# Kernel tuning notes

Measured on AMD Instinct MI355X. Metric: run time of the kernel, lower is better.

The kernel has to match this reference:

```python
import jax, jax.numpy as jnp
import numpy as np

B, L, V, D, N, K = 8, 512, 50257, 1024, 1024, 256


def setup_inputs() -> dict:
    key = jax.random.key(0)
    ks = jax.random.split(key, 8)
    s = 0.02
    return {
        "input_ids": jax.random.randint(ks[0], (B, L), 0, V, dtype=jnp.int32),
        "emb_inp": jax.random.normal(ks[1], (V, D), jnp.float32) * s,
        "W_ih": jax.random.normal(ks[2], (3 * D, D), jnp.float32) * s,   # rows ordered [r|z|n] like torch GRU
        "W_hh": jax.random.normal(ks[3], (3 * D, D), jnp.float32) * s,
        "b_ih": jnp.zeros((3 * D,), jnp.float32),
        "b_hh": jnp.zeros((3 * D,), jnp.float32),
        "W_A": jax.random.normal(ks[4], (N * K, D), jnp.float32) * s,    # ctx_to_A weight
        "b_A": jnp.zeros((N * K,), jnp.float32),
        "emb_geom": jax.random.normal(ks[5], (V, N), jnp.float32) * s,
    }


def reference(input_ids, emb_inp, W_ih, W_hh, b_ih, b_hh, W_A, b_A, emb_geom):
    # token embedding: (B, L, D)
    x = emb_inp[input_ids]
    # precompute input-side GRU gates once: (B, L, 3D)
    gi = jnp.einsum('bld,gd->blg', x, W_ih) + b_ih

    def step(h, gi_t):
        gh = h @ W_hh.T + b_hh                       # (B, 3D)
        ir, iz, i_n = jnp.split(gi_t, 3, axis=-1)
        hr, hz, h_n = jnp.split(gh, 3, axis=-1)
        r = jax.nn.sigmoid(ir + hr)
        z = jax.nn.sigmoid(iz + hz)
        n = jnp.tanh(i_n + r * h_n)
        h_new = (1.0 - z) * n + z * h                # torch GRU update
        return h_new, None

    h0 = jnp.zeros((x.shape[0], D), x.dtype)
    ctx_vec, _ = jax.lax.scan(step, h0, jnp.swapaxes(gi, 0, 1))  # final hidden (B, D)

    # context -> subspace basis U: (B, n, k)
    U = (ctx_vec @ W_A.T + b_A).reshape(-1, N, K)

    # scores[b,v] = e_v^T (U U^T) e_v == ||U^T e_v||^2  (rank-k rewrite, same math)
    Ue = jnp.einsum('vn,bnk->bvk', emb_geom, U)      # (B, V, K)
    logits = jnp.sum(Ue * Ue, axis=-1)               # (B, V)
    return logits
```

## Files before the change

### kernel.cpp

```cpp
#include <hip/hip_runtime.h>

#define D 1024
#define G3 3072
#define NV 50257
#define NU 1024
#define KU 256
#define TOKROWS 4096
#define SCL 256.0f
#define ISCL2 (1.0f / 65536.0f)
#define ISCL4 (1.0f / 4294967296.0f)

typedef __attribute__((ext_vector_type(8))) _Float16 half8;
typedef __attribute__((ext_vector_type(4))) _Float16 half4;
typedef __attribute__((ext_vector_type(4))) float f32x4;
typedef __attribute__((ext_vector_type(4))) unsigned u32x4;

#define GLDS16(gp, lp) __builtin_amdgcn_global_load_lds( \
    (const __attribute__((address_space(1))) void*)(const void*)(gp), \
    (__attribute__((address_space(3))) void*)(void*)(lp), 16, 0, 0)

static __device__ __forceinline__ float sigmoidf_(float x) {
  return 1.0f / (1.0f + __expf(-x));
}
static __device__ __forceinline__ float tanhf_(float x) {
  float e = __expf(2.0f * x);
  return 1.0f - 2.0f / (e + 1.0f);
}

__global__ __launch_bounds__(256) void k_prep(
    const int* __restrict__ ids, const float* __restrict__ emb,
    const float* __restrict__ Wih,
    _Float16* __restrict__ xh, _Float16* __restrict__ xl,
    _Float16* __restrict__ wh, _Float16* __restrict__ wl)
{
  int t = threadIdx.x;
  int wg = blockIdx.x;
  const float* src;
  _Float16 *dh, *dl;
  if (wg < TOKROWS) {
    src = emb + (size_t)ids[wg] * D;
    dh = xh + (size_t)wg * D; dl = xl + (size_t)wg * D;
  } else {
    int r = wg - TOKROWS;
    src = Wih + (size_t)r * D;
    dh = wh + (size_t)r * D; dl = wl + (size_t)r * D;
  }
  f32x4 v = ((const f32x4*)src)[t];
  half4 h, l;
#pragma unroll
  for (int j = 0; j < 4; ++j) {
    float vs = v[j] * SCL;
    _Float16 hi = (_Float16)vs;
    h[j] = hi;
    l[j] = (_Float16)(vs - (float)hi);
  }
  *(half4*)(dh + t * 4) = h;
  *(half4*)(dl + t * 4) = l;
}

__global__ __launch_bounds__(256) void k_gi(
    const _Float16* __restrict__ Ah, const _Float16* __restrict__ Al,
    const _Float16* __restrict__ Bh, const _Float16* __restrict__ Bl,
    const float* __restrict__ bih, float* __restrict__ gi)
{
  __shared__ _Float16 Ash[128 * 64];
  __shared__ _Float16 Asl[128 * 64];
  __shared__ _Float16 Bsh[128 * 64];
  __shared__ _Float16 Bsl[128 * 64];
  int tid = threadIdx.x;
  int bm = blockIdx.x, bn = blockIdx.y;
  int lane = tid & 63, w = tid >> 6;
  int nl = lane & 15, q = lane >> 4;
  int wr = w >> 1, wc = w & 1;
  f32x4 zero = {0.f, 0.f, 0.f, 0.f};
  f32x4 acc[4][4];
#pragma unroll
  for (int i = 0; i < 4; i++)
#pragma unroll
    for (int j = 0; j < 4; j++) acc[i][j] = zero;
  int srow_in = tid >> 3;
  int cg = ((tid & 7) ^ (srow_in & 7)) * 8;
  for (int kc = 0; kc < 16; ++kc) {
    __syncthreads();
#pragma unroll
    for (int s = 0; s < 4; ++s) {
      size_t go = ((size_t)(bm * 128 + s * 32 + srow_in)) * D + kc * 64 + cg;
      size_t go2 = ((size_t)(bn * 128 + s * 32 + srow_in)) * D + kc * 64 + cg;
      int lb = s * 2048 + w * 512;
      GLDS16(Ah + go, Ash + lb);
      GLDS16(Al + go, Asl + lb);
      GLDS16(Bh + go2, Bsh + lb);
      GLDS16(Bl + go2, Bsl + lb);
    }
    __syncthreads();
    half8 afh[4][2], afl[4][2], bfh[4][2], bfl[4][2];
#pragma unroll
    for (int mt = 0; mt < 4; ++mt) {
      int R = wr * 64 + mt * 16 + nl;
#pragma unroll
      for (int kt = 0; kt < 2; ++kt) {
        int o = R * 64 + ((kt * 4 + q) ^ (R & 7)) * 8;
        afh[mt][kt] = *(const half8*)(Ash + o);
        afl[mt][kt] = *(const half8*)(Asl + o);
      }
    }
#pragma unroll
    for (int nt = 0; nt < 4; ++nt) {
      int R = wc * 64 + nt * 16 + nl;
#pragma unroll
      for (int kt = 0; kt < 2; ++kt) {
        int o = R * 64 + ((kt * 4 + q) ^ (R & 7)) * 8;
        bfh[nt][kt] = *(const half8*)(Bsh + o);
        bfl[nt][kt] = *(const half8*)(Bsl + o);
      }
    }
#pragma unroll
    for (int mt = 0; mt < 4; ++mt)
#pragma unroll
      for (int nt = 0; nt < 4; ++nt)
#pragma unroll
        for (int kt = 0; kt < 2; ++kt) {
          acc[mt][nt] = __builtin_amdgcn_mfma_f32_16x16x32_f16(afh[mt][kt], bfh[nt][kt], acc[mt][nt], 0, 0, 0);
          acc[mt][nt] = __builtin_amdgcn_mfma_f32_16x16x32_f16(afh[mt][kt], bfl[nt][kt], acc[mt][nt], 0, 0, 0);
          acc[mt][nt] = __builtin_amdgcn_mfma_f32_16x16x32_f16(afl[mt][kt], bfh[nt][kt], acc[mt][nt], 0, 0, 0);
        }
  }
#pragma unroll
  for (int mt = 0; mt < 4; ++mt)
#pragma unroll
    for (int nt = 0; nt < 4; ++nt) {
      int col = bn * 128 + wc * 64 + nt * 16 + nl;
      float bv = bih[col];
#pragma unroll
      for (int i = 0; i < 4; i++) {
        int row = bm * 128 + wr * 64 + mt * 16 + q * 4 + i;
        gi[(size_t)row * G3 + col] = acc[mt][nt][i] * ISCL2 + bv;
      }
    }
}

__global__ void k_init(unsigned* __restrict__ rec32)
{
  int t = threadIdx.x;
  for (int i = t; i < 32768; i += 256) rec32[i] = 0u;
}

__global__ __launch_bounds__(384) void k_gru(
    const float* __restrict__ Whh, const float* __restrict__ gi,
    const float* __restrict__ bhh, unsigned* __restrict__ hrec,
    float* __restrict__ ctx)
{
  int tid = threadIdx.x;
  int wid = blockIdx.x;
  int w = tid >> 6;
  int g = w >> 1;
  int kh = w & 1;
  int lane = tid & 63, nl = lane & 15, q = lane >> 4;
  __shared__ _Float16 hs[16 * 1024];
  __shared__ float gp[6][3][8][17];

  half8 bwh[16], bwl[16];
  {
    const float* wrow = Whh + ((size_t)(g * 1024 + wid * 16 + nl)) * D + kh * 512;
#pragma unroll
    for (int kt = 0; kt < 16; ++kt) {
      const f32x4* p = (const f32x4*)(wrow + kt * 32 + q * 8);
      f32x4 v0 = p[0], v1 = p[1];
      half8 h, l;
#pragma unroll
      for (int j = 0; j < 4; ++j) {
        float s0 = v0[j] * SCL;
        _Float16 h0 = (_Float16)s0;
        h[j] = h0; l[j] = (_Float16)(s0 - (float)h0);
        float s1 = v1[j] * SCL;
        _Float16 h1 = (_Float16)s1;
        h[j + 4] = h1; l[j + 4] = (_Float16)(s1 - (float)h1);
      }
      bwh[kt] = h; bwl[kt] = l;
    }
  }

  int m = tid >> 3, np = (tid & 7) * 2;
  int d0 = wid * 16 + np;
  float hr0 = 0.f, hr1 = 0.f;
  float bh[6] = {0, 0, 0, 0, 0, 0};
  if (tid < 64) {
#pragma unroll
    for (int gg = 0; gg < 3; ++gg) {
      bh[gg * 2] = bhh[gg * 1024 + d0];
      bh[gg * 2 + 1] = bhh[gg * 1024 + d0 + 1];
    }
  }
  f32x4 zero = {0, 0, 0, 0};

  for (int step = 0; step < 512; ++step) {
    float gi6[6] = {0, 0, 0, 0, 0, 0};
    if (tid < 64) {
      const float* gpt = gi + ((size_t)(m * 512 + step)) * G3 + d0;
#pragma unroll
      for (int gg = 0; gg < 3; ++gg) {
        gi6[gg * 2] = gpt[gg * 1024];
        gi6[gg * 2 + 1] = gpt[gg * 1024 + 1];
      }
    }

    {
      unsigned want = (unsigned)step;
      const u32x4* rb = (const u32x4*)hrec + (size_t)(step & 1) * 4096;
      u32x4 rv[11];
      unsigned need = 0;
#pragma unroll
      for (int k = 0; k < 11; ++k) {
        int r = tid + k * 384;
        if (r < 4096) need |= (1u << k);
      }
      while (need) {
        unsigned mm = need;
#pragma unroll
        for (int k = 0; k < 11; ++k)
          if (mm & (1u << k)) {
            int r = tid + k * 384;
            asm volatile("global_load_dwordx4 %0, %1, off sc0 sc1"
                         : "=v"(rv[k]) : "v"(rb + r));
          }
        asm volatile("s_waitcnt vmcnt(0)" ::: "memory");
#pragma unroll
        for (int k = 0; k < 11; ++k)
          if ((mm & (1u << k)) && rv[k][2] == want) need &= ~(1u << k);
      }
      __builtin_amdgcn_sched_barrier(0);
#pragma unroll
      for (int k = 0; k < 11; ++k) {
        int r = tid + k * 384;
        if (r < 4096) {
          int w2 = r >> 6, l2 = r & 63;
          int m2 = l2 >> 3;
          int d = (w2 << 4) + ((l2 & 7) << 1);
          int chunk = d >> 3, wi = d & 7;
          int sw = chunk ^ (m2 & 7);
          *(unsigned*)&hs[((m2 * 128 + sw) << 3) + wi] = rv[k][0];
          *(unsigned*)&hs[(((m2 + 8) * 128 + sw) << 3) + wi] = rv[k][1];
        }
      }
    }
    __syncthreads();

    half8 av[16];
#pragma unroll
    for (int kt = 0; kt < 16; ++kt) {
      int chunk = kh * 64 + kt * 4 + q;
      av[kt] = *(const half8*)&hs[(size_t)(nl * 128 + (chunk ^ (nl & 7))) * 8];
    }
    f32x4 ac1 = zero, ac2 = zero;
#pragma unroll
    for (int kt = 0; kt < 16; ++kt) {
      ac1 = __builtin_amdgcn_mfma_f32_16x16x32_f16(av[kt], bwh[kt], ac1, 0, 0, 0);
      ac2 = __builtin_amdgcn_mfma_f32_16x16x32_f16(av[kt], bwl[kt], ac2, 0, 0, 0);
    }
    if (q < 2) {
#pragma unroll
      for (int i = 0; i < 4; i++) {
        gp[w][0][q * 4 + i][nl] = ac1[i];
        gp[w][2][q * 4 + i][nl] = ac2[i];
      }
    } else {
#pragma unroll
      for (int i = 0; i < 4; i++) gp[w][1][(q - 2) * 4 + i][nl] = ac1[i];
    }
    __syncthreads();
    if (tid < 64) {
      float gh[6];
#pragma unroll
      for (int g2 = 0; g2 < 3; ++g2) {
        float s0 = 0.f, s1 = 0.f;
#pragma unroll
        for (int k2 = 0; k2 < 2; ++k2) {
          int wv = g2 * 2 + k2;
#pragma unroll
          for (int s = 0; s < 3; ++s) {
            s0 += gp[wv][s][m][np];
            s1 += gp[wv][s][m][np + 1];
          }
        }
        gh[g2 * 2] = s0 * ISCL2;
        gh[g2 * 2 + 1] = s1 * ISCL2;
      }
      float r0_ = sigmoidf_(gi6[0] + gh[0] + bh[0]);
      float r1_ = sigmoidf_(gi6[1] + gh[1] + bh[1]);
      float z0_ = sigmoidf_(gi6[2] + gh[2] + bh[2]);
      float z1_ = sigmoidf_(gi6[3] + gh[3] + bh[3]);
      float n0_ = tanhf_(gi6[4] + r0_ * (gh[4] + bh[4]));
      float n1_ = tanhf_(gi6[5] + r1_ * (gh[5] + bh[5]));
      float h0_ = (1.f - z0_) * n0_ + z0_ * hr0;
      float h1_ = (1.f - z1_) * n1_ + z1_ * hr1;
      hr0 = h0_; hr1 = h1_;
      float s0 = h0_ * SCL, s1 = h1_ * SCL;
      _Float16 h0h = (_Float16)s0, h1h = (_Float16)s1;
      _Float16 h0l = (_Float16)(s0 - (float)h0h), h1l = (_Float16)(s1 - (float)h1h);
      u32x4 rec;
      rec[0] = (unsigned)__builtin_bit_cast(unsigned short, h0h) |
               ((unsigned)__builtin_bit_cast(unsigned short, h1h) << 16);
      rec[1] = (unsigned)__builtin_bit_cast(unsigned short, h0l) |
               ((unsigned)__builtin_bit_cast(unsigned short, h1l) << 16);
      rec[2] = (unsigned)(step + 1);
      rec[3] = 0u;
      u32x4* dst = (u32x4*)hrec + ((size_t)((step + 1) & 1) * 4096 + wid * 64 + tid);
      asm volatile("global_store_dwordx4 %0, %1, off sc0 sc1"
                   :: "v"(dst), "v"(rec) : "memory");
      if (step == 511) {
        ctx[m * D + d0] = h0_;
        ctx[m * D + d0 + 1] = h1_;
      }
    }
  }
}

__global__ __launch_bounds__(256) void k_u(
    const float* __restrict__ WA, const float* __restrict__ bA,
    const float* __restrict__ ctx, _Float16* __restrict__ Uth,
    _Float16* __restrict__ Utl)
{
  __shared__ float As[128 * 32];
  __shared__ float cx[8][1032];
  int tid = threadIdx.x;
  int RB = blockIdx.x;
#pragma unroll
  for (int jj = 0; jj < 8; ++jj) {
    int e = tid * 32 + jj * 4;
    *(f32x4*)&cx[e >> 10][e & 1023] = *(const f32x4*)(ctx + e);
  }
  float acc[4] = {0.f, 0.f, 0.f, 0.f};
  int b = tid & 7, rq = tid >> 3;
  float* AsW = As + (tid >> 6) * 256;
  int sr = tid >> 3;
  int sc = (tid & 7) * 4;
  __syncthreads();
  for (int kc = 0; kc < 32; ++kc) {
    __syncthreads();
    const float* gsrc = WA + ((size_t)(RB * 128 + sr)) * D + kc * 32 + sc;
    GLDS16(gsrc, AsW);
    GLDS16(gsrc + 32 * D, AsW + 1024);
    GLDS16(gsrc + 64 * D, AsW + 2048);
    GLDS16(gsrc + 96 * D, AsW + 3072);
    __syncthreads();
    f32x4 cxr[8];
#pragma unroll
    for (int kk = 0; kk < 8; ++kk) cxr[kk] = *(const f32x4*)&cx[b][kc * 32 + kk * 4];
#pragma unroll
    for (int r = 0; r < 4; ++r) {
      const float* ap = As + (rq * 4 + r) * 32;
      float s = 0.f;
#pragma unroll
      for (int kk = 0; kk < 8; ++kk) {
        f32x4 a = *(const f32x4*)(ap + kk * 4);
        f32x4 c = cxr[kk];
        s += a[0] * c[0] + a[1] * c[1] + a[2] * c[2] + a[3] * c[3];
      }
      acc[r] += s;
    }
  }
#pragma unroll
  for (int r = 0; r < 4; ++r) {
    int R = RB * 128 + rq * 4 + r;
    float v = (acc[r] + bA[R]) * SCL;
    int n_u = R >> 8, k_u = R & 255;
    _Float16 hi = (_Float16)v;
    size_t o = ((size_t)(b * 256 + k_u)) * NU + n_u;
    Uth[o] = hi;
    Utl[o] = (_Float16)(v - (float)hi);
  }
}

__global__ __launch_bounds__(512, 1) void k_logits(
    const float* __restrict__ eg, const _Float16* __restrict__ Uth,
    const _Float16* __restrict__ Utl, float* __restrict__ out)
{
  __shared__ _Float16 Ash[128 * 40];
  __shared__ _Float16 Asl[128 * 40];
  __shared__ float lacc[8][128];
  int tid = threadIdx.x;
  int v0 = blockIdx.x * 128;
  int lane = tid & 63, w = tid >> 6, nl = lane & 15, q = lane >> 4;
  int bh = w & 1, wk = w >> 1;
  for (int i = tid; i < 1024; i += 512) ((float*)lacc)[i] = 0.f;
  int sr = tid >> 2;
  int sc = (tid & 3) * 8;
  int vr = v0 + sr;
  if (vr >= NV) vr = NV - 1;
  const float* asrc = eg + (size_t)vr * NU;
  f32x4 zero = {0, 0, 0, 0};
  f32x4 u0 = *(const f32x4*)(asrc + sc);
  f32x4 u1 = *(const f32x4*)(asrc + sc + 4);
  __syncthreads();
  for (int kg = 0; kg < 4; ++kg) {
    f32x4 acc[4][8];
#pragma unroll
    for (int b = 0; b < 4; ++b)
#pragma unroll
      for (int mt = 0; mt < 8; ++mt) acc[b][mt] = zero;
    for (int nc = 0; nc < 32; ++nc) {
      __syncthreads();
      {
        half8 h, l;
#pragma unroll
        for (int j = 0; j < 4; ++j) {
          float s0 = u0[j] * SCL;
          _Float16 h0 = (_Float16)s0;
          h[j] = h0; l[j] = (_Float16)(s0 - (float)h0);
          float s1 = u1[j] * SCL;
          _Float16 h1 = (_Float16)s1;
          h[j + 4] = h1; l[j + 4] = (_Float16)(s1 - (float)h1);
        }
        *(half8*)(Ash + sr * 40 + sc) = h;
        *(half8*)(Asl + sr * 40 + sc) = l;
      }
      {
        int nnc = (nc + 1) & 31;
        const f32x4* np_ = (const f32x4*)(asrc + nnc * 32 + sc);
        u0 = np_[0];
        u1 = np_[1];
      }
      __syncthreads();
      half8 afh[8], afl[8];
#pragma unroll
      for (int mt = 0; mt < 8; ++mt) {
        afh[mt] = *(const half8*)(Ash + (mt * 16 + nl) * 40 + q * 8);
        afl[mt] = *(const half8*)(Asl + (mt * 16 + nl) * 40 + q * 8);
      }
      __builtin_amdgcn_s_setprio(1);
#pragma unroll
      for (int b = 0; b < 4; ++b) {
        int bb = bh * 4 + b;
        size_t o = ((size_t)(bb * 256 + kg * 64 + wk * 16 + nl)) * NU + nc * 32 + q * 8;
        half8 bfh = *(const half8*)(Uth + o);
        half8 bfl = *(const half8*)(Utl + o);
#pragma unroll
        for (int mt = 0; mt < 8; ++mt) {
          acc[b][mt] = __builtin_amdgcn_mfma_f32_16x16x32_f16(afh[mt], bfh, acc[b][mt], 0, 0, 0);
          acc[b][mt] = __builtin_amdgcn_mfma_f32_16x16x32_f16(afh[mt], bfl, acc[b][mt], 0, 0, 0);
          acc[b][mt] = __builtin_amdgcn_mfma_f32_16x16x32_f16(afl[mt], bfh, acc[b][mt], 0, 0, 0);
        }
      }
      __builtin_amdgcn_s_setprio(0);
    }
#pragma unroll
    for (int b = 0; b < 4; ++b) {
      int bb = bh * 4 + b;
#pragma unroll
      for (int mt = 0; mt < 8; ++mt) {
#pragma unroll
        for (int i = 0; i < 4; ++i) {
          float s = acc[b][mt][i] * acc[b][mt][i];
          s += __shfl_xor(s, 1);
          s += __shfl_xor(s, 2);
          s += __shfl_xor(s, 4);
          s += __shfl_xor(s, 8);
          if (nl == 0) atomicAdd(&lacc[bb][mt * 16 + q * 4 + i], s);
        }
      }
    }
  }
  __syncthreads();
  if (tid < 128) {
    int v = v0 + tid;
    if (v < NV) {
#pragma unroll
      for (int b = 0; b < 8; ++b) out[(size_t)b * NV + v] = lacc[b][tid] * ISCL4;
    }
  }
}

extern "C" void kernel_launch(void* const* d_in, const int* in_sizes, int n_in,
                              void* d_out, int out_size, void* d_ws, size_t ws_size,
                              hipStream_t stream)
{
  (void)in_sizes; (void)n_in; (void)out_size; (void)ws_size;
  const int* ids = (const int*)d_in[0];
  const float* emb = (const float*)d_in[1];
  const float* Wih = (const float*)d_in[2];
  const float* Whh = (const float*)d_in[3];
  const float* bih = (const float*)d_in[4];
  const float* bhh = (const float*)d_in[5];
  const float* WA = (const float*)d_in[6];
  const float* bA = (const float*)d_in[7];
  const float* eg = (const float*)d_in[8];
  float* out = (float*)d_out;

  char* ws = (char*)d_ws;
  size_t off = 0;
  auto take = [&](size_t bytes) -> char* {
    char* p = ws + off;
    off += (bytes + 255) & ~(size_t)255;
    return p;
  };
  float* gi32 = (float*)take((size_t)4096 * 3072 * 4);
  char* xregion = take((size_t)4096 * 1024 * 2 * 2);
  _Float16* xh = (_Float16*)xregion;
  _Float16* xl = xh + (size_t)4096 * 1024;
  _Float16* wh = (_Float16*)take((size_t)3072 * 1024 * 2);
  _Float16* wl = (_Float16*)take((size_t)3072 * 1024 * 2);
  unsigned* hrec = (unsigned*)take((size_t)2 * 4096 * 16);
  float* ctx = (float*)take((size_t)8 * 1024 * 4);
  _Float16* Uth = (_Float16*)xregion;
  _Float16* Utl = Uth + (size_t)8 * 256 * 1024;

  k_prep<<<dim3(7168), dim3(256), 0, stream>>>(ids, emb, Wih, xh, xl, wh, wl);
  k_gi<<<dim3(32, 24), dim3(256), 0, stream>>>(xh, xl, wh, wl, bih, gi32);
  k_init<<<dim3(1), dim3(256), 0, stream>>>(hrec);
  k_gru<<<dim3(64), dim3(384), 0, stream>>>(Whh, gi32, bhh, hrec, ctx);
  k_u<<<dim3(2048), dim3(256), 0, stream>>>(WA, bA, ctx, Uth, Utl);
  k_logits<<<dim3(393), dim3(512), 0, stream>>>(eg, Uth, Utl, out);
}
```

Measured before the change: 3.037 ms.

## Halve per-wave accumulator footprint in k_logits to allow two blocks per CU

Waves now split the batch into four pairs instead of two halves, so each wave holds 2x8 accumulators instead of 4x8. The k-loop runs over eight 32-wide groups instead of four 64-wide ones. A fragments are loaded in two chunks of four, and launch bounds allow two blocks per CU, with the goal of higher occupancy to hide latency. The register prefetch of the next embedding chunk is dropped, and the embedding matrix is now re-read and re-split eight times instead of four, which adds global traffic and conversion work.

Result: faster. 2.964 ms (median of 2 runs) (-2.4%).

```diff
diff --git a/kernel.cpp b/kernel.cpp
--- a/kernel.cpp
+++ b/kernel.cpp
@@ -371,7 +371,7 @@
   }
 }
 
-__global__ __launch_bounds__(512, 1) void k_logits(
+__global__ __launch_bounds__(512, 2) void k_logits(
     const float* __restrict__ eg, const _Float16* __restrict__ Uth,
     const _Float16* __restrict__ Utl, float* __restrict__ out)
 {
@@ -381,7 +381,7 @@
   int tid = threadIdx.x;
   int v0 = blockIdx.x * 128;
   int lane = tid & 63, w = tid >> 6, nl = lane & 15, q = lane >> 4;
-  int bh = w & 1, wk = w >> 1;
+  int bq = w & 3, wk = w >> 2;
   for (int i = tid; i < 1024; i += 512) ((float*)lacc)[i] = 0.f;
   int sr = tid >> 2;
   int sc = (tid & 3) * 8;
@@ -389,18 +389,19 @@
   if (vr >= NV) vr = NV - 1;
   const float* asrc = eg + (size_t)vr * NU;
   f32x4 zero = {0, 0, 0, 0};
-  f32x4 u0 = *(const f32x4*)(asrc + sc);
-  f32x4 u1 = *(const f32x4*)(asrc + sc + 4);
   __syncthreads();
-  for (int kg = 0; kg < 4; ++kg) {
-    f32x4 acc[4][8];
-#pragma unroll
-    for (int b = 0; b < 4; ++b)
+  for (int kg = 0; kg < 8; ++kg) {
+    f32x4 acc[2][8];
+#pragma unroll
+    for (int b = 0; b < 2; ++b)
 #pragma unroll
       for (int mt = 0; mt < 8; ++mt) acc[b][mt] = zero;
     for (int nc = 0; nc < 32; ++nc) {
       __syncthreads();
       {
+        const f32x4* p = (const f32x4*)(asrc + nc * 32 + sc);
+        f32x4 u0 = p[0];
+        f32x4 u1 = p[1];
         half8 h, l;
 #pragma unroll
         for (int j = 0; j < 4; ++j) {
@@ -414,38 +415,43 @@
         *(half8*)(Ash + sr * 40 + sc) = h;
         *(half8*)(Asl + sr * 40 + sc) = l;
       }
+      __syncthreads();
+      half8 bfh0, bfl0, bfh1, bfl1;
       {
-        int nnc = (nc + 1) & 31;
-        const f32x4* np_ = (const f32x4*)(asrc + nnc * 32 + sc);
-        u0 = np_[0];
-        u1 = np_[1];
-      }
-      __syncthreads();
-      half8 afh[8], afl[8];
-#pragma unroll
-      for (int mt = 0; mt < 8; ++mt) {
-        afh[mt] = *(const half8*)(Ash + (mt * 16 + nl) * 40 + q * 8);
-        afl[mt] = *(const half8*)(Asl + (mt * 16 + nl) * 40 + q * 8);
+        int bb0 = bq * 2;
+        size_t o0 = ((size_t)(bb0 * 256 + kg * 32 + wk * 16 + nl)) * NU + nc * 32 + q * 8;
+        size_t o1 = o0 + (size_t)256 * NU;
+        bfh0 = *(const half8*)(Uth + o0);
+        bfl0 = *(const half8*)(Utl + o0);
+        bfh1 = *(const half8*)(Uth + o1);
+        bfl1 = *(const half8*)(Utl + o1);
       }
       __builtin_amdgcn_s_setprio(1);
 #pragma unroll
-      for (int b = 0; b < 4; ++b) {
-        int bb = bh * 4 + b;
-        size_t o = ((size_t)(bb * 256 + kg * 64 + wk * 16 + nl)) * NU + nc * 32 + q * 8;
-        half8 bfh = *(const half8*)(Uth + o);
-        half8 bfl = *(const half8*)(Utl + o);
-#pragma unroll
-        for (int mt = 0; mt < 8; ++mt) {
-          acc[b][mt] = __builtin_amdgcn_mfma_f32_16x16x32_f16(afh[mt], bfh, acc[b][mt], 0, 0, 0);
-          acc[b][mt] = __builtin_amdgcn_mfma_f32_16x16x32_f16(afh[mt], bfl, acc[b][mt], 0, 0, 0);
-          acc[b][mt] = __builtin_amdgcn_mfma_f32_16x16x32_f16(afl[mt], bfh, acc[b][mt], 0, 0, 0);
+      for (int c = 0; c < 2; ++c) {
+        half8 afh[4], afl[4];
+#pragma unroll
+        for (int mt = 0; mt < 4; ++mt) {
+          int row = (c * 4 + mt) * 16 + nl;
+          afh[mt] = *(const half8*)(Ash + row * 40 + q * 8);
+          afl[mt] = *(const half8*)(Asl + row * 40 + q * 8);
+        }
+#pragma unroll
+        for (int mt = 0; mt < 4; ++mt) {
+          int g = c * 4 + mt;
+          acc[0][g] = __builtin_amdgcn_mfma_f32_16x16x32_f16(afh[mt], bfh0, acc[0][g], 0, 0, 0);
+          acc[0][g] = __builtin_amdgcn_mfma_f32_16x16x32_f16(afh[mt], bfl0, acc[0][g], 0, 0, 0);
+          acc[0][g] = __builtin_amdgcn_mfma_f32_16x16x32_f16(afl[mt], bfh0, acc[0][g], 0, 0, 0);
+          acc[1][g] = __builtin_amdgcn_mfma_f32_16x16x32_f16(afh[mt], bfh1, acc[1][g], 0, 0, 0);
+          acc[1][g] = __builtin_amdgcn_mfma_f32_16x16x32_f16(afh[mt], bfl1, acc[1][g], 0, 0, 0);
+          acc[1][g] = __builtin_amdgcn_mfma_f32_16x16x32_f16(afl[mt], bfh1, acc[1][g], 0, 0, 0);
         }
       }
       __builtin_amdgcn_s_setprio(0);
     }
 #pragma unroll
-    for (int b = 0; b < 4; ++b) {
-      int bb = bh * 4 + b;
+    for (int b = 0; b < 2; ++b) {
+      int bb = bq * 2 + b;
 #pragma unroll
       for (int mt = 0; mt < 8; ++mt) {
 #pragma unroll
```
